# Performance work log

Hardware: AMD Instinct MI355X
Metric: run time of the kernel (lower is better)

Reference implementation:

```python
import jax, jax.numpy as jnp
import numpy as np

N_NODES = 100000
N_EDGES = 1600000
IN_F = 256
OUT_F = 128


def setup_inputs() -> dict:
    key = jax.random.key(0)
    k_x, k_w, k_r, k_c, k_v = jax.random.split(key, 5)
    x = jax.random.normal(k_x, (N_NODES, IN_F), dtype=jnp.float32)
    weight = jax.random.normal(k_w, (IN_F, OUT_F), dtype=jnp.float32) * (1.0 / np.sqrt(IN_F))
    edge_row = jax.random.randint(k_r, (N_EDGES,), 0, N_NODES, dtype=jnp.int32)
    edge_col = jax.random.randint(k_c, (N_EDGES,), 0, N_NODES, dtype=jnp.int32)
    edge_vals = jax.random.uniform(k_v, (N_EDGES,), dtype=jnp.float32)
    return {"x": x, "weight": weight, "edge_row": edge_row,
            "edge_col": edge_col, "edge_vals": edge_vals}


def reference(x, weight, edge_row, edge_col, edge_vals):
    # Dense projection: h = x @ W  (torch: self.linear(x), bias=False)
    h = x @ weight                                   # [N, OUT_F]
    # SpMM: out[i] = sum_{(i,j) in E} A_hat[i,j] * h[j]
    messages = edge_vals[:, None] * h[edge_col]      # [E, OUT_F] gather
    out = jax.ops.segment_sum(messages, edge_row, num_segments=N_NODES)
    return out
```

## Files before the change

### kernel.cpp

```cpp
#include <hip/hip_runtime.h>
#include <hip/hip_bf16.h>


#define IN_F  256
#define OUT_F 128
#define BSH   6
#define CH    4096
#define CAP   1536

typedef __attribute__((ext_vector_type(8))) short sh8;
typedef __attribute__((ext_vector_type(4))) float f32x4;

__device__ __forceinline__ unsigned short f2bf(float f) {
    unsigned u = __float_as_uint(f);
    unsigned r = u + 0x7fff + ((u >> 16) & 1);
    return (unsigned short)(r >> 16);
}
__device__ __forceinline__ float bf2f(unsigned short s) {
    return __uint_as_float(((unsigned)s) << 16);
}

__global__ __launch_bounds__(256) void wt_prep_kernel(
    const float* __restrict__ w, unsigned short* __restrict__ wt) {
    int i = blockIdx.x * 256 + threadIdx.x;
    int k = i >> 7, n = i & 127;
    wt[n * IN_F + k] = f2bf(w[i]);
}

__global__ __launch_bounds__(256) void gemm_mfma_kernel(
    const float* __restrict__ x, const unsigned short* __restrict__ wt,
    unsigned short* __restrict__ h, int n_nodes) {
    int tid = threadIdx.x;
    int wv = tid >> 6, l = tid & 63;
    int l16 = l & 15, lk = (l >> 4) * 8;
    int ch = blockIdx.y;
    long row0 = (long)blockIdx.x * 128 + wv * 32;

    long rmax = n_nodes - 1;
    long ra0 = row0 + l16;      if (ra0 > rmax) ra0 = rmax;
    long ra1 = row0 + 16 + l16; if (ra1 > rmax) ra1 = rmax;
    const float* xp0 = x + ra0 * IN_F + lk;
    const float* xp1 = x + ra1 * IN_F + lk;
    const unsigned short* wp = wt + (ch * 64 + l16) * IN_F + lk;

    f32x4 acc[2][4];
    #pragma unroll
    for (int rt = 0; rt < 2; rt++)
        #pragma unroll
        for (int nt = 0; nt < 4; nt++)
            acc[rt][nt] = (f32x4){0.f, 0.f, 0.f, 0.f};

    #pragma unroll
    for (int ks = 0; ks < 8; ks++) {
        int k0 = ks * 32;
        float4 t0 = *(const float4*)(xp0 + k0);
        float4 t1 = *(const float4*)(xp0 + k0 + 4);
        float4 t2 = *(const float4*)(xp1 + k0);
        float4 t3 = *(const float4*)(xp1 + k0 + 4);
        sh8 a0, a1;
        a0[0] = (short)f2bf(t0.x); a0[1] = (short)f2bf(t0.y);
        a0[2] = (short)f2bf(t0.z); a0[3] = (short)f2bf(t0.w);
        a0[4] = (short)f2bf(t1.x); a0[5] = (short)f2bf(t1.y);
        a0[6] = (short)f2bf(t1.z); a0[7] = (short)f2bf(t1.w);
        a1[0] = (short)f2bf(t2.x); a1[1] = (short)f2bf(t2.y);
        a1[2] = (short)f2bf(t2.z); a1[3] = (short)f2bf(t2.w);
        a1[4] = (short)f2bf(t3.x); a1[5] = (short)f2bf(t3.y);
        a1[6] = (short)f2bf(t3.z); a1[7] = (short)f2bf(t3.w);
        #pragma unroll
        for (int nt = 0; nt < 4; nt++) {
            sh8 b = *(const sh8*)(wp + nt * 16 * IN_F + k0);
            acc[0][nt] = __builtin_amdgcn_mfma_f32_16x16x32_bf16(
                a0, b, acc[0][nt], 0, 0, 0);
            acc[1][nt] = __builtin_amdgcn_mfma_f32_16x16x32_bf16(
                a1, b, acc[1][nt], 0, 0, 0);
        }
    }

    int rbase = (l >> 4) * 4;
    #pragma unroll
    for (int rt = 0; rt < 2; rt++) {
        #pragma unroll
        for (int j = 0; j < 4; j++) {
            long r = row0 + rt * 16 + rbase + j;
            if (r < n_nodes) {
                unsigned short* hp = h + r * OUT_F + ch * 64 + l16;
                #pragma unroll
                for (int nt = 0; nt < 4; nt++)
                    hp[nt * 16] = f2bf(acc[rt][nt][j]);
            }
        }
    }
}

__global__ __launch_bounds__(256) void hist_kernel(
    const int* __restrict__ erow, int* __restrict__ T,
    int n_edges, int nbuck) {
    __shared__ int lh[2048];
    int tid = threadIdx.x, b = blockIdx.x;
    for (int k = tid; k < nbuck; k += 256) lh[k] = 0;
    __syncthreads();
    int s = b * CH, e = min(s + CH, n_edges);
    for (int i = s + tid; i < e; i += 256)
        atomicAdd(&lh[erow[i] >> BSH], 1);
    __syncthreads();
    int* Tr = T + (long)b * nbuck;
    for (int k = tid; k < nbuck; k += 256) Tr[k] = lh[k];
}

__global__ __launch_bounds__(256) void colscan_kernel(
    int* __restrict__ T, int* __restrict__ colTotal, int nblk, int nbuck) {
    int k = blockIdx.x * 4 + (threadIdx.x >> 6);
    int lane = threadIdx.x & 63;
    if (k >= nbuck) return;
    int carry = 0;
    for (int c = 0; c < nblk; c += 64) {
        int b = c + lane;
        int v = (b < nblk) ? T[(long)b * nbuck + k] : 0;
        int incl = v;
        #pragma unroll
        for (int off = 1; off < 64; off <<= 1) {
            int t = __shfl_up(incl, off);
            if (lane >= off) incl += t;
        }
        if (b < nblk) T[(long)b * nbuck + k] = carry + incl - v;
        carry += __shfl(incl, 63);
    }
    if (lane == 0) colTotal[k] = carry;
}

__global__ __launch_bounds__(256) void basescan_kernel(
    const int* __restrict__ colTotal, int* __restrict__ base, int nbuck) {
    __shared__ int s[256];
    int tid = threadIdx.x;
    int loc[8];
    int sum = 0;
    #pragma unroll
    for (int j = 0; j < 8; j++) {
        int i = tid * 8 + j;
        loc[j] = (i < nbuck) ? colTotal[i] : 0;
        sum += loc[j];
    }
    s[tid] = sum;
    __syncthreads();
    for (int off = 1; off < 256; off <<= 1) {
        int t = (tid >= off) ? s[tid - off] : 0;
        __syncthreads();
        s[tid] += t;
        __syncthreads();
    }
    int pre = s[tid] - sum;
    #pragma unroll
    for (int j = 0; j < 8; j++) {
        int i = tid * 8 + j;
        if (i < nbuck) base[i] = pre;
        pre += loc[j];
    }
    if (tid == 255) base[nbuck] = pre;
}

__global__ __launch_bounds__(256) void scatter_kernel(
    const int* __restrict__ erow, const int* __restrict__ ecol,
    const float* __restrict__ eval, const int* __restrict__ T,
    const int* __restrict__ base, unsigned long long* __restrict__ epack,
    int n_edges, int nbuck) {
    __shared__ int lpos[2048];
    int tid = threadIdx.x, b = blockIdx.x;
    const int* Tr = T + (long)b * nbuck;
    for (int k = tid; k < nbuck; k += 256) lpos[k] = base[k] + Tr[k];
    __syncthreads();
    int s = b * CH, e = min(s + CH, n_edges);
    for (int i = s + tid; i < e; i += 256) {
        int r = erow[i];
        int c = ecol[i];
        float v = eval[i];
        int p = atomicAdd(&lpos[r >> BSH], 1);
        epack[p] = ((unsigned long long)__float_as_uint(v) << 32)
                 | ((unsigned)(r & 63) << 17) | (unsigned)c;
    }
}

__global__ __launch_bounds__(256) void bucket_rowsum_kernel(
    const unsigned short* __restrict__ h, const int* __restrict__ base,
    const unsigned long long* __restrict__ epack,
    float* __restrict__ out, int n_nodes, int nbuck) {
    __shared__ unsigned long long sorted[CAP];
    __shared__ int lh[64], lo[64], lc[64];
    int tid = threadIdx.x, k = blockIdx.x;
    int s = base[k], e = base[k + 1];
    int size = e - s;
    int wv = tid >> 6, lane = tid & 63;

    if (tid < 64) { lh[tid] = 0; lc[tid] = 0; }
    __syncthreads();
    for (int i = tid; i < size; i += 256) {
        unsigned lo32 = (unsigned)(epack[s + i] & 0xffffffffu);
        atomicAdd(&lh[(lo32 >> 17) & 63], 1);
    }
    __syncthreads();
    if (tid < 64) {
        int v = lh[tid];
        int incl = v;
        #pragma unroll
        for (int off = 1; off < 64; off <<= 1) {
            int t = __shfl_up(incl, off);
            if (lane >= off) incl += t;
        }
        lo[tid] = incl - v;
    }
    __syncthreads();
    bool fits = (size <= CAP);
    if (fits) {
        for (int i = tid; i < size; i += 256) {
            unsigned long long ed = epack[s + i];
            int r = (int)((ed >> 17) & 63);
            int p = atomicAdd(&lc[r], 1) + lo[r];
            sorted[p] = ed;
        }
    }
    __syncthreads();

#define GSTEP(EV)                                                            \
    {                                                                        \
        unsigned hv = *((const unsigned*)(h + (long)((EV) & 0x1ffffu) * OUT_F) + lane); \
        float vv = __uint_as_float((unsigned)((EV) >> 32));                  \
        a0 += vv * bf2f((unsigned short)(hv & 0xffff));                      \
        a1 += vv * bf2f((unsigned short)(hv >> 16));                         \
    }

    for (int rr = 0; rr < 16; rr++) {
        int r = wv * 16 + rr;
        long row = (long)k * 64 + r;
        if (row >= n_nodes) break;
        int rs = lo[r], cnt = lh[r];
        float a0 = 0.f, a1 = 0.f;
        if (fits) {
            int j = 0;
            for (; j + 8 <= cnt; j += 8) {
                unsigned long long e0 = sorted[rs + j];
                unsigned long long e1 = sorted[rs + j + 1];
                unsigned long long e2 = sorted[rs + j + 2];
                unsigned long long e3 = sorted[rs + j + 3];
                unsigned long long e4 = sorted[rs + j + 4];
                unsigned long long e5 = sorted[rs + j + 5];
                unsigned long long e6 = sorted[rs + j + 6];
                unsigned long long e7 = sorted[rs + j + 7];
                GSTEP(e0) GSTEP(e1) GSTEP(e2) GSTEP(e3)
                GSTEP(e4) GSTEP(e5) GSTEP(e6) GSTEP(e7)
            }
            for (; j + 4 <= cnt; j += 4) {
                unsigned long long e0 = sorted[rs + j];
                unsigned long long e1 = sorted[rs + j + 1];
                unsigned long long e2 = sorted[rs + j + 2];
                unsigned long long e3 = sorted[rs + j + 3];
                GSTEP(e0) GSTEP(e1) GSTEP(e2) GSTEP(e3)
            }
            for (; j < cnt; j++) {
                unsigned long long e0 = sorted[rs + j];
                GSTEP(e0)
            }
        } else {
            for (int i = 0; i < size; i++) {
                unsigned long long ed = epack[s + i];
                if ((int)((ed >> 17) & 63) == r) GSTEP(ed)
            }
        }
        float2 o; o.x = a0; o.y = a1;
        *(float2*)(out + row * OUT_F + lane * 2) = o;
    }
#undef GSTEP
}

extern "C" void kernel_launch(void* const* d_in, const int* in_sizes, int n_in,
                              void* d_out, int out_size, void* d_ws, size_t ws_size,
                              hipStream_t stream) {
    const float* x    = (const float*)d_in[0];
    const float* w    = (const float*)d_in[1];
    const int*   erow = (const int*)d_in[2];
    const int*   ecol = (const int*)d_in[3];
    const float* eval = (const float*)d_in[4];
    float* out = (float*)d_out;

    int n_nodes = in_sizes[0] / IN_F;
    int n_edges = in_sizes[2];
    int nbuck = (n_nodes + 63) >> BSH;
    int nblk  = (n_edges + CH - 1) / CH;

    char* p = (char*)d_ws;
    auto alloc = [&](size_t bytes) {
        char* q = p;
        p += (bytes + 255) & ~(size_t)255;
        return q;
    };
    unsigned short* h  = (unsigned short*)alloc((size_t)n_nodes * OUT_F * 2);
    int* T        = (int*)alloc((size_t)nblk * nbuck * 4);
    int* colTotal = (int*)alloc((size_t)nbuck * 4);
    int* base     = (int*)alloc((size_t)(nbuck + 1) * 4);
    unsigned long long* epack = (unsigned long long*)alloc((size_t)n_edges * 8);
    unsigned short* wt = (unsigned short*)alloc((size_t)IN_F * OUT_F * 2);

    wt_prep_kernel<<<dim3((IN_F * OUT_F) / 256), 256, 0, stream>>>(w, wt);
    gemm_mfma_kernel<<<dim3((n_nodes + 127) / 128, 2), 256, 0, stream>>>(
        x, wt, h, n_nodes);

    hist_kernel<<<dim3(nblk), 256, 0, stream>>>(erow, T, n_edges, nbuck);
    colscan_kernel<<<dim3((nbuck + 3) / 4), 256, 0, stream>>>(
        T, colTotal, nblk, nbuck);
    basescan_kernel<<<dim3(1), 256, 0, stream>>>(colTotal, base, nbuck);
    scatter_kernel<<<dim3(nblk), 256, 0, stream>>>(
        erow, ecol, eval, T, base, epack, n_edges, nbuck);

    bucket_rowsum_kernel<<<dim3(nbuck), 256, 0, stream>>>(
        h, base, epack, out, n_nodes, nbuck);
}
```

Baseline: 168.7 us.

## Stage x tile in LDS as bf16 and compute all output columns per block

The GEMM previously launched two column-halves per row tile, so each block read its x rows from global memory and converted them to bf16 twice. Now each block loads a 64-row x tile once with coalesced float4 loads, converts it to bf16 in padded shared memory, and each wave computes 16 rows across all 128 output columns. This halves global reads of x and removes the duplicated conversion. In exchange it adds an LDS round-trip and a barrier, and each thread keeps more accumulator registers, which may lower occupancy.

```diff
diff --git a/kernel.cpp b/kernel.cpp
--- a/kernel.cpp
+++ b/kernel.cpp
@@ -7,6 +7,7 @@
 #define BSH   6
 #define CH    4096
 #define CAP   1536
+#define XLS   264
 
 typedef __attribute__((ext_vector_type(8))) short sh8;
 typedef __attribute__((ext_vector_type(4))) float f32x4;
@@ -30,64 +31,53 @@
 __global__ __launch_bounds__(256) void gemm_mfma_kernel(
     const float* __restrict__ x, const unsigned short* __restrict__ wt,
     unsigned short* __restrict__ h, int n_nodes) {
+    __shared__ unsigned short xs[64 * XLS];
     int tid = threadIdx.x;
-    int wv = tid >> 6, l = tid & 63;
-    int l16 = l & 15, lk = (l >> 4) * 8;
-    int ch = blockIdx.y;
-    long row0 = (long)blockIdx.x * 128 + wv * 32;
-
+    int w = tid >> 6, lane = tid & 63;
+    long blk0 = (long)blockIdx.x * 64;
     long rmax = n_nodes - 1;
-    long ra0 = row0 + l16;      if (ra0 > rmax) ra0 = rmax;
-    long ra1 = row0 + 16 + l16; if (ra1 > rmax) ra1 = rmax;
-    const float* xp0 = x + ra0 * IN_F + lk;
-    const float* xp1 = x + ra1 * IN_F + lk;
-    const unsigned short* wp = wt + (ch * 64 + l16) * IN_F + lk;
-
-    f32x4 acc[2][4];
-    #pragma unroll
-    for (int rt = 0; rt < 2; rt++)
-        #pragma unroll
-        for (int nt = 0; nt < 4; nt++)
-            acc[rt][nt] = (f32x4){0.f, 0.f, 0.f, 0.f};
+
+    #pragma unroll
+    for (int it = 0; it < 16; it++) {
+        int row = it * 4 + w;
+        long grow = blk0 + row; if (grow > rmax) grow = rmax;
+        float4 t = *(const float4*)(x + grow * IN_F + lane * 4);
+        ushort4 o;
+        o.x = f2bf(t.x); o.y = f2bf(t.y); o.z = f2bf(t.z); o.w = f2bf(t.w);
+        *(ushort4*)(xs + row * XLS + lane * 4) = o;
+    }
+    __syncthreads();
+
+    int l16 = lane & 15, hi = lane >> 4, lk = hi * 8;
+    const unsigned short* xrow = xs + (w * 16 + l16) * XLS;
+    const unsigned short* wp = wt + l16 * IN_F + lk;
+
+    f32x4 acc[8];
+    #pragma unroll
+    for (int nt = 0; nt < 8; nt++)
+        acc[nt] = (f32x4){0.f, 0.f, 0.f, 0.f};
 
     #pragma unroll
     for (int ks = 0; ks < 8; ks++) {
         int k0 = ks * 32;
-        float4 t0 = *(const float4*)(xp0 + k0);
-        float4 t1 = *(const float4*)(xp0 + k0 + 4);
-        float4 t2 = *(const float4*)(xp1 + k0);
-        float4 t3 = *(const float4*)(xp1 + k0 + 4);
-        sh8 a0, a1;
-        a0[0] = (short)f2bf(t0.x); a0[1] = (short)f2bf(t0.y);
-        a0[2] = (short)f2bf(t0.z); a0[3] = (short)f2bf(t0.w);
-        a0[4] = (short)f2bf(t1.x); a0[5] = (short)f2bf(t1.y);
-        a0[6] = (short)f2bf(t1.z); a0[7] = (short)f2bf(t1.w);
-        a1[0] = (short)f2bf(t2.x); a1[1] = (short)f2bf(t2.y);
-        a1[2] = (short)f2bf(t2.z); a1[3] = (short)f2bf(t2.w);
-        a1[4] = (short)f2bf(t3.x); a1[5] = (short)f2bf(t3.y);
-        a1[6] = (short)f2bf(t3.z); a1[7] = (short)f2bf(t3.w);
+        sh8 a = *(const sh8*)(xrow + k0 + lk);
         #pragma unroll
-        for (int nt = 0; nt < 4; nt++) {
+        for (int nt = 0; nt < 8; nt++) {
             sh8 b = *(const sh8*)(wp + nt * 16 * IN_F + k0);
-            acc[0][nt] = __builtin_amdgcn_mfma_f32_16x16x32_bf16(
-                a0, b, acc[0][nt], 0, 0, 0);
-            acc[1][nt] = __builtin_amdgcn_mfma_f32_16x16x32_bf16(
-                a1, b, acc[1][nt], 0, 0, 0);
-        }
-    }
-
-    int rbase = (l >> 4) * 4;
-    #pragma unroll
-    for (int rt = 0; rt < 2; rt++) {
-        #pragma unroll
-        for (int j = 0; j < 4; j++) {
-            long r = row0 + rt * 16 + rbase + j;
-            if (r < n_nodes) {
-                unsigned short* hp = h + r * OUT_F + ch * 64 + l16;
-                #pragma unroll
-                for (int nt = 0; nt < 4; nt++)
-                    hp[nt * 16] = f2bf(acc[rt][nt][j]);
-            }
+            acc[nt] = __builtin_amdgcn_mfma_f32_16x16x32_bf16(
+                a, b, acc[nt], 0, 0, 0);
+        }
+    }
+
+    int rbase = hi * 4;
+    #pragma unroll
+    for (int j = 0; j < 4; j++) {
+        long r = blk0 + w * 16 + rbase + j;
+        if (r < n_nodes) {
+            unsigned short* hp = h + r * OUT_F + l16;
+            #pragma unroll
+            for (int nt = 0; nt < 8; nt++)
+                hp[nt * 16] = f2bf(acc[nt][j]);
         }
     }
 }
@@ -299,7 +289,7 @@
     unsigned short* wt = (unsigned short*)alloc((size_t)IN_F * OUT_F * 2);
 
     wt_prep_kernel<<<dim3((IN_F * OUT_F) / 256), 256, 0, stream>>>(w, wt);
-    gemm_mfma_kernel<<<dim3((n_nodes + 127) / 128, 2), 256, 0, stream>>>(
+    gemm_mfma_kernel<<<dim3((n_nodes + 63) / 64), 256, 0, stream>>>(
         x, wt, h, n_nodes);
 
     hist_kernel<<<dim3(nblk), 256, 0, stream>>>(erow, T, n_edges, nbuck);
```

Result: slower. 176.1 us (+4.4%).

## Compute full 128-column GEMM tile per block with swapped MFMA operands

Applied to the files above, without the earlier changes.

The GEMM grid drops its second dimension, so each block computes all 128 output columns instead of one 64-column half. The x rows are loaded and converted to bf16 once rather than twice across two blocks. The MFMA operands are swapped (weights as A, x as B), which transposes the accumulator layout so each lane holds four consecutive columns of one row. That allows vectorized ushort4 stores instead of scattered 2-byte stores. In exchange the accumulator count doubles to 64 floats per thread, raising register pressure and possibly lowering occupancy.

```diff
diff --git a/kernel.cpp b/kernel.cpp
--- a/kernel.cpp
+++ b/kernel.cpp
@@ -32,8 +32,7 @@
     unsigned short* __restrict__ h, int n_nodes) {
     int tid = threadIdx.x;
     int wv = tid >> 6, l = tid & 63;
-    int l16 = l & 15, lk = (l >> 4) * 8;
-    int ch = blockIdx.y;
+    int l16 = l & 15, hi = l >> 4, lk = hi * 8;
     long row0 = (long)blockIdx.x * 128 + wv * 32;
 
     long rmax = n_nodes - 1;
@@ -41,13 +40,13 @@
     long ra1 = row0 + 16 + l16; if (ra1 > rmax) ra1 = rmax;
     const float* xp0 = x + ra0 * IN_F + lk;
     const float* xp1 = x + ra1 * IN_F + lk;
-    const unsigned short* wp = wt + (ch * 64 + l16) * IN_F + lk;
-
-    f32x4 acc[2][4];
+    const unsigned short* wp = wt + l16 * IN_F + lk;
+
+    f32x4 acc[2][8];
     #pragma unroll
     for (int rt = 0; rt < 2; rt++)
         #pragma unroll
-        for (int nt = 0; nt < 4; nt++)
+        for (int nt = 0; nt < 8; nt++)
             acc[rt][nt] = (f32x4){0.f, 0.f, 0.f, 0.f};
 
     #pragma unroll
@@ -57,36 +56,38 @@
         float4 t1 = *(const float4*)(xp0 + k0 + 4);
         float4 t2 = *(const float4*)(xp1 + k0);
         float4 t3 = *(const float4*)(xp1 + k0 + 4);
-        sh8 a0, a1;
-        a0[0] = (short)f2bf(t0.x); a0[1] = (short)f2bf(t0.y);
-        a0[2] = (short)f2bf(t0.z); a0[3] = (short)f2bf(t0.w);
-        a0[4] = (short)f2bf(t1.x); a0[5] = (short)f2bf(t1.y);
-        a0[6] = (short)f2bf(t1.z); a0[7] = (short)f2bf(t1.w);
-        a1[0] = (short)f2bf(t2.x); a1[1] = (short)f2bf(t2.y);
-        a1[2] = (short)f2bf(t2.z); a1[3] = (short)f2bf(t2.w);
-        a1[4] = (short)f2bf(t3.x); a1[5] = (short)f2bf(t3.y);
-        a1[6] = (short)f2bf(t3.z); a1[7] = (short)f2bf(t3.w);
+        sh8 xb0, xb1;
+        xb0[0] = (short)f2bf(t0.x); xb0[1] = (short)f2bf(t0.y);
+        xb0[2] = (short)f2bf(t0.z); xb0[3] = (short)f2bf(t0.w);
+        xb0[4] = (short)f2bf(t1.x); xb0[5] = (short)f2bf(t1.y);
+        xb0[6] = (short)f2bf(t1.z); xb0[7] = (short)f2bf(t1.w);
+        xb1[0] = (short)f2bf(t2.x); xb1[1] = (short)f2bf(t2.y);
+        xb1[2] = (short)f2bf(t2.z); xb1[3] = (short)f2bf(t2.w);
+        xb1[4] = (short)f2bf(t3.x); xb1[5] = (short)f2bf(t3.y);
+        xb1[6] = (short)f2bf(t3.z); xb1[7] = (short)f2bf(t3.w);
         #pragma unroll
-        for (int nt = 0; nt < 4; nt++) {
-            sh8 b = *(const sh8*)(wp + nt * 16 * IN_F + k0);
+        for (int nt = 0; nt < 8; nt++) {
+            sh8 aw = *(const sh8*)(wp + nt * 16 * IN_F + k0);
             acc[0][nt] = __builtin_amdgcn_mfma_f32_16x16x32_bf16(
-                a0, b, acc[0][nt], 0, 0, 0);
+                aw, xb0, acc[0][nt], 0, 0, 0);
             acc[1][nt] = __builtin_amdgcn_mfma_f32_16x16x32_bf16(
-                a1, b, acc[1][nt], 0, 0, 0);
-        }
-    }
-
-    int rbase = (l >> 4) * 4;
+                aw, xb1, acc[1][nt], 0, 0, 0);
+        }
+    }
+
     #pragma unroll
     for (int rt = 0; rt < 2; rt++) {
-        #pragma unroll
-        for (int j = 0; j < 4; j++) {
-            long r = row0 + rt * 16 + rbase + j;
-            if (r < n_nodes) {
-                unsigned short* hp = h + r * OUT_F + ch * 64 + l16;
-                #pragma unroll
-                for (int nt = 0; nt < 4; nt++)
-                    hp[nt * 16] = f2bf(acc[rt][nt][j]);
+        long row = row0 + rt * 16 + l16;
+        if (row < n_nodes) {
+            unsigned short* hp = h + row * OUT_F + hi * 4;
+            #pragma unroll
+            for (int nt = 0; nt < 8; nt++) {
+                ushort4 o;
+                o.x = f2bf(acc[rt][nt][0]);
+                o.y = f2bf(acc[rt][nt][1]);
+                o.z = f2bf(acc[rt][nt][2]);
+                o.w = f2bf(acc[rt][nt][3]);
+                *(ushort4*)(hp + nt * 16) = o;
             }
         }
     }
@@ -299,7 +300,7 @@
     unsigned short* wt = (unsigned short*)alloc((size_t)IN_F * OUT_F * 2);
 
     wt_prep_kernel<<<dim3((IN_F * OUT_F) / 256), 256, 0, stream>>>(w, wt);
-    gemm_mfma_kernel<<<dim3((n_nodes + 127) / 128, 2), 256, 0, stream>>>(
+    gemm_mfma_kernel<<<dim3((n_nodes + 127) / 128), 256, 0, stream>>>(
         x, wt, h, n_nodes);
 
     hist_kernel<<<dim3(nblk), 256, 0, stream>>>(erow, T, n_edges, nbuck);
```

Result: no change. 167.8 us (-0.5%).

## Fuse row histogram into GEMM launch with interleaved block roles

Applied to the files above, without the earlier changes.

Merges the edge-row histogram kernel into the MFMA GEMM kernel as one launch. Histogram blocks are interleaved every R blocks among GEMM tiles so the atomic-heavy histogram work overlaps with the compute- and bandwidth-bound projection. This removes one launch and its tail. In exchange, the GEMM blocks now reserve the 8KB shared histogram array, which may reduce occupancy, and the block-index arithmetic becomes more complex.

```diff
diff --git a/kernel.cpp b/kernel.cpp
--- a/kernel.cpp
+++ b/kernel.cpp
@@ -27,14 +27,38 @@
     wt[n * IN_F + k] = f2bf(w[i]);
 }
 
-__global__ __launch_bounds__(256) void gemm_mfma_kernel(
+__global__ __launch_bounds__(256) void fused_gemm_hist_kernel(
     const float* __restrict__ x, const unsigned short* __restrict__ wt,
-    unsigned short* __restrict__ h, int n_nodes) {
-    int tid = threadIdx.x;
+    unsigned short* __restrict__ h, int n_nodes,
+    const int* __restrict__ erow, int* __restrict__ T,
+    int n_edges, int nbuck, int nblk, int nrow_tiles, int R) {
+    __shared__ int lh[2048];
+    int g = blockIdx.x, tid = threadIdx.x;
+    int hq = g / R;
+    bool is_hist = ((g % R) == 0) && (hq < nblk);
+
+    if (is_hist) {
+        int b = hq;
+        for (int k = tid; k < nbuck; k += 256) lh[k] = 0;
+        __syncthreads();
+        int s = b * CH, e = min(s + CH, n_edges);
+        for (int i = s + tid; i < e; i += 256)
+            atomicAdd(&lh[erow[i] >> BSH], 1);
+        __syncthreads();
+        int* Tr = T + (long)b * nbuck;
+        for (int k = tid; k < nbuck; k += 256) Tr[k] = lh[k];
+        return;
+    }
+
+    int nhist_before = min(hq + ((g % R) ? 1 : 0), nblk);
+    int gemm_idx = g - nhist_before;
+    int rt_idx = gemm_idx % nrow_tiles;
+    int ch = gemm_idx / nrow_tiles;
+    if (ch > 1) return;
+
     int wv = tid >> 6, l = tid & 63;
     int l16 = l & 15, lk = (l >> 4) * 8;
-    int ch = blockIdx.y;
-    long row0 = (long)blockIdx.x * 128 + wv * 32;
+    long row0 = (long)rt_idx * 128 + wv * 32;
 
     long rmax = n_nodes - 1;
     long ra0 = row0 + l16;      if (ra0 > rmax) ra0 = rmax;
@@ -90,21 +114,6 @@
             }
         }
     }
-}
-
-__global__ __launch_bounds__(256) void hist_kernel(
-    const int* __restrict__ erow, int* __restrict__ T,
-    int n_edges, int nbuck) {
-    __shared__ int lh[2048];
-    int tid = threadIdx.x, b = blockIdx.x;
-    for (int k = tid; k < nbuck; k += 256) lh[k] = 0;
-    __syncthreads();
-    int s = b * CH, e = min(s + CH, n_edges);
-    for (int i = s + tid; i < e; i += 256)
-        atomicAdd(&lh[erow[i] >> BSH], 1);
-    __syncthreads();
-    int* Tr = T + (long)b * nbuck;
-    for (int k = tid; k < nbuck; k += 256) Tr[k] = lh[k];
 }
 
 __global__ __launch_bounds__(256) void colscan_kernel(
@@ -299,10 +308,14 @@
     unsigned short* wt = (unsigned short*)alloc((size_t)IN_F * OUT_F * 2);
 
     wt_prep_kernel<<<dim3((IN_F * OUT_F) / 256), 256, 0, stream>>>(w, wt);
-    gemm_mfma_kernel<<<dim3((n_nodes + 127) / 128, 2), 256, 0, stream>>>(
-        x, wt, h, n_nodes);
-
-    hist_kernel<<<dim3(nblk), 256, 0, stream>>>(erow, T, n_edges, nbuck);
+
+    int nrow_tiles = (n_nodes + 127) / 128;
+    int ngemm = nrow_tiles * 2;
+    int total = ngemm + nblk;
+    int R = (total + nblk - 1) / nblk;
+    fused_gemm_hist_kernel<<<dim3(total), 256, 0, stream>>>(
+        x, wt, h, n_nodes, erow, T, n_edges, nbuck, nblk, nrow_tiles, R);
+
     colscan_kernel<<<dim3((nbuck + 3) / 4), 256, 0, stream>>>(
         T, colTotal, nblk, nbuck);
     basescan_kernel<<<dim3(1), 256, 0, stream>>>(colTotal, base, nbuck);
```

New measurement: 164.7 us. 2.3% less time.
